# Kernel optimization log

Measured on AMD Instinct MI355X. Metric: run time of the kernel, lower is better.

The kernel has to match this reference:

```python
import jax, jax.numpy as jnp
import numpy as np

B, N, NBR, C = 1, 2048, 32, 384
C1, OUT = 32, 128


def setup_inputs() -> dict:
    key = jax.random.key(0)
    ks = jax.random.split(key, 6)
    return {
        "s_i": jax.random.normal(ks[0], (B, N, C), dtype=jnp.float32),
        "s_j": jax.random.normal(ks[1], (B, N, NBR, C), dtype=jnp.float32),
        "m_i": jnp.ones((B, N), dtype=jnp.float32),
        "m_j": jnp.ones((B, N, NBR), dtype=jnp.float32),
        "Wl": jax.random.normal(ks[2], (C, C1), dtype=jnp.float32) * (C ** -0.5),
        "bl": jnp.zeros((C1,), dtype=jnp.float32),
        "Wr": jax.random.normal(ks[3], (C, C1), dtype=jnp.float32) * (C ** -0.5),
        "br": jnp.zeros((C1,), dtype=jnp.float32),
        "Wo": jax.random.normal(ks[4], (C1 * C1, OUT), dtype=jnp.float32) * ((C1 * C1) ** -0.5),
        "bo": jnp.zeros((OUT,), dtype=jnp.float32),
    }


def reference(s_i, s_j, m_i, m_j, Wl, bl, Wr, br, Wo, bo):
    # Masked projections
    left = m_i[..., None] * (jnp.einsum('bic,ca->bia', s_i, Wl) + bl)      # (B, N, C1)
    right = m_j[..., None] * (jnp.einsum('bikc,ca->bika', s_j, Wr) + br)   # (B, N, n, C1)
    # Per-(residue, neighbor) outer product; equals the repeat/reshape/transpose
    # dance in the original: out[b,i,k,a*C1+c] = left[b,i,a] * right[b,i,k,c]
    op = jnp.einsum('bia,bikc->bikac', left, right)                        # (B, N, n, C1, C1)
    b_, n_, k_ = op.shape[:3]
    op = op.reshape(b_, n_, k_, C1 * C1)
    # Output projection
    return jnp.einsum('bikd,do->biko', op, Wo) + bo                        # (B, N, n, OUT)
```

## Files before the change

### kernel.cpp

```cpp
#include <hip/hip_runtime.h>

constexpr int NRES = 2048;
constexpr int NBR  = 32;
constexpr int C    = 384;
constexpr int C1   = 32;
constexpr int OUTD = 128;

constexpr int CHUNK = 64;
constexpr int NCH   = C / CHUNK;
constexpr int SJ_LD = CHUNK + 4;

__global__ __launch_bounds__(256, 4) void outerprod_kernel(
    const float* __restrict__ s_i, const float* __restrict__ s_j,
    const float* __restrict__ m_i, const float* __restrict__ m_j,
    const float* __restrict__ Wl,  const float* __restrict__ bl,
    const float* __restrict__ Wr,  const float* __restrict__ br,
    const float* __restrict__ Wo,  const float* __restrict__ bo,
    float* __restrict__ out)
{
    const int i = blockIdx.x;
    const int t = threadIdx.x;

    __shared__ float red[8][C1];
    __shared__ float lft[C1];
    __shared__ float rgt[NBR * C1];
    __shared__ float Tm[C1 * OUTD];
    __shared__ float sj[2][NBR * SJ_LD];

    const int f0 = t,        kk0 = f0 >> 4, c40 = (f0 & 15) * 4;
    const int f1 = t + 256,  kk1 = f1 >> 4, c41 = (f1 & 15) * 4;
    const float* sjbase = s_j + (size_t)i * NBR * C;

    float4 st0 = *reinterpret_cast<const float4*>(sjbase + kk0 * C + c40);
    float4 st1 = *reinterpret_cast<const float4*>(sjbase + kk1 * C + c41);

    {
        const int a = t & 31, g = t >> 5;
        const float* si = s_i + (size_t)i * C;
        const int c0 = g * 48;
        float acc = 0.f;
        #pragma unroll 4
        for (int c = c0; c < c0 + 48; c += 4) {
            const float4 s4 = *reinterpret_cast<const float4*>(si + c);
            acc = fmaf(s4.x, Wl[(c + 0) * C1 + a], acc);
            acc = fmaf(s4.y, Wl[(c + 1) * C1 + a], acc);
            acc = fmaf(s4.z, Wl[(c + 2) * C1 + a], acc);
            acc = fmaf(s4.w, Wl[(c + 3) * C1 + a], acc);
        }
        red[g][a] = acc;
    }
    __syncthreads();

    *reinterpret_cast<float4*>(&sj[0][kk0 * SJ_LD + c40]) = st0;
    *reinterpret_cast<float4*>(&sj[0][kk1 * SJ_LD + c41]) = st1;

    if (t < C1) {
        float acc = bl[t];
        #pragma unroll
        for (int g = 0; g < 8; ++g) acc += red[g][t];
        lft[t] = m_i[i] * acc;
    }

    const int k = t >> 3, cg = t & 7;
    float acc0 = 0.f, acc1 = 0.f, acc2 = 0.f, acc3 = 0.f;
    int cur = 0;
    for (int ch = 0; ch < NCH; ++ch) {
        if (ch + 1 < NCH) {
            st0 = *reinterpret_cast<const float4*>(sjbase + kk0 * C + (ch + 1) * CHUNK + c40);
            st1 = *reinterpret_cast<const float4*>(sjbase + kk1 * C + (ch + 1) * CHUNK + c41);
        }
        __syncthreads();

        const float* srow  = &sj[cur][k * SJ_LD];
        const float* wbase = Wr + (size_t)(ch * CHUNK) * C1 + cg * 4;
        #pragma unroll
        for (int c4 = 0; c4 < CHUNK / 4; ++c4) {
            const float4 s4 = *reinterpret_cast<const float4*>(srow + c4 * 4);
            float4 w;
            w = *reinterpret_cast<const float4*>(wbase + (c4 * 4 + 0) * C1);
            acc0 = fmaf(s4.x, w.x, acc0); acc1 = fmaf(s4.x, w.y, acc1);
            acc2 = fmaf(s4.x, w.z, acc2); acc3 = fmaf(s4.x, w.w, acc3);
            w = *reinterpret_cast<const float4*>(wbase + (c4 * 4 + 1) * C1);
            acc0 = fmaf(s4.y, w.x, acc0); acc1 = fmaf(s4.y, w.y, acc1);
            acc2 = fmaf(s4.y, w.z, acc2); acc3 = fmaf(s4.y, w.w, acc3);
            w = *reinterpret_cast<const float4*>(wbase + (c4 * 4 + 2) * C1);
            acc0 = fmaf(s4.z, w.x, acc0); acc1 = fmaf(s4.z, w.y, acc1);
            acc2 = fmaf(s4.z, w.z, acc2); acc3 = fmaf(s4.z, w.w, acc3);
            w = *reinterpret_cast<const float4*>(wbase + (c4 * 4 + 3) * C1);
            acc0 = fmaf(s4.w, w.x, acc0); acc1 = fmaf(s4.w, w.y, acc1);
            acc2 = fmaf(s4.w, w.z, acc2); acc3 = fmaf(s4.w, w.w, acc3);
        }

        if (ch + 1 < NCH) {
            *reinterpret_cast<float4*>(&sj[cur ^ 1][kk0 * SJ_LD + c40]) = st0;
            *reinterpret_cast<float4*>(&sj[cur ^ 1][kk1 * SJ_LD + c41]) = st1;
        }
        cur ^= 1;
    }
    {
        const float  m  = m_j[i * NBR + k];
        const float4 b4 = *reinterpret_cast<const float4*>(br + cg * 4);
        rgt[k * C1 + cg * 4 + 0] = m * (acc0 + b4.x);
        rgt[k * C1 + cg * 4 + 1] = m * (acc1 + b4.y);
        rgt[k * C1 + cg * 4 + 2] = m * (acc2 + b4.z);
        rgt[k * C1 + cg * 4 + 3] = m * (acc3 + b4.w);
    }
    __syncthreads();

    #pragma unroll
    for (int j = 0; j < 4; ++j) {
        const int e4 = t + j * 256;
        const int c  = e4 >> 5;
        const int o  = (e4 & 31) * 4;
        float a0 = 0.f, a1 = 0.f, a2 = 0.f, a3 = 0.f;
        #pragma unroll 8
        for (int a = 0; a < C1; ++a) {
            const float  l  = lft[a];
            const float4 w4 = *reinterpret_cast<const float4*>(
                Wo + ((size_t)(a * C1 + c)) * OUTD + o);
            a0 = fmaf(l, w4.x, a0); a1 = fmaf(l, w4.y, a1);
            a2 = fmaf(l, w4.z, a2); a3 = fmaf(l, w4.w, a3);
        }
        float4 r = {a0, a1, a2, a3};
        *reinterpret_cast<float4*>(&Tm[c * OUTD + o]) = r;
    }
    __syncthreads();

    #pragma unroll
    for (int j = 0; j < 4; ++j) {
        const int e4 = t + j * 256;
        const int kk = e4 >> 5;
        const int o  = (e4 & 31) * 4;
        const float4 b4 = *reinterpret_cast<const float4*>(bo + o);
        float a0 = b4.x, a1 = b4.y, a2 = b4.z, a3 = b4.w;
        #pragma unroll 8
        for (int c = 0; c < C1; ++c) {
            const float  r  = rgt[kk * C1 + c];
            const float4 tv = *reinterpret_cast<const float4*>(&Tm[c * OUTD + o]);
            a0 = fmaf(r, tv.x, a0); a1 = fmaf(r, tv.y, a1);
            a2 = fmaf(r, tv.z, a2); a3 = fmaf(r, tv.w, a3);
        }
        const float4 res = {a0, a1, a2, a3};
        *reinterpret_cast<float4*>(&out[((size_t)i * NBR + kk) * OUTD + o]) = res;
    }
}

extern "C" void kernel_launch(void* const* d_in, const int* in_sizes, int n_in,
                              void* d_out, int out_size, void* d_ws, size_t ws_size,
                              hipStream_t stream) {
    (void)in_sizes; (void)n_in; (void)out_size; (void)d_ws; (void)ws_size;
    const float* s_i = (const float*)d_in[0];
    const float* s_j = (const float*)d_in[1];
    const float* m_i = (const float*)d_in[2];
    const float* m_j = (const float*)d_in[3];
    const float* Wl  = (const float*)d_in[4];
    const float* bl  = (const float*)d_in[5];
    const float* Wr  = (const float*)d_in[6];
    const float* br  = (const float*)d_in[7];
    const float* Wo  = (const float*)d_in[8];
    const float* bo  = (const float*)d_in[9];
    float* out = (float*)d_out;

    outerprod_kernel<<<NRES, 256, 0, stream>>>(
        s_i, s_j, m_i, m_j, Wl, bl, Wr, br, Wo, bo, out);
}
```

Before: 317.9 us.

## Split fused kernel into projection, T-matrix GEMM, and output kernels via workspace

Replaces the single per-residue fused kernel with three kernels. The first computes the left and right projections over 128-row tiles, using a swizzled shared-memory layout and storing right transposed. The second computes the per-residue T = L·Wo as a register-tiled GEMM so Wo is reused across 64 residues. The third combines R with T to produce the output. The goal is to stop every block re-reading the whole 512KB Wo. The cost is a 32MB T intermediate round-tripped through global memory plus extra launches, and the path depends on the workspace being large enough, with the old kernel kept as a fallback.

```diff
diff --git a/kernel.cpp b/kernel.cpp
--- a/kernel.cpp
+++ b/kernel.cpp
@@ -5,12 +5,181 @@
 constexpr int C    = 384;
 constexpr int C1   = 32;
 constexpr int OUTD = 128;
-
-constexpr int CHUNK = 64;
-constexpr int NCH   = C / CHUNK;
-constexpr int SJ_LD = CHUNK + 4;
-
-__global__ __launch_bounds__(256, 4) void outerprod_kernel(
+constexpr int M1   = NRES * NBR;
+
+constexpr size_t R_OFF = 0;
+constexpr size_t L_OFF = (size_t)8 << 20;
+constexpr size_t T_OFF = (size_t)9 << 20;
+constexpr size_t WS_NEED = T_OFF + (size_t)NRES * (C1 * OUTD) * sizeof(float);
+
+__global__ __launch_bounds__(256) void k1_proj(
+    const float* __restrict__ s_i, const float* __restrict__ s_j,
+    const float* __restrict__ m_i, const float* __restrict__ m_j,
+    const float* __restrict__ Wl,  const float* __restrict__ bl,
+    const float* __restrict__ Wr,  const float* __restrict__ br,
+    float* __restrict__ Rt, float* __restrict__ Lg)
+{
+    const int b    = blockIdx.x;
+    const int t    = threadIdx.x;
+    const int lane = t & 63;
+    const int n0   = __builtin_amdgcn_readfirstlane((t >> 6) * 8);
+
+    __shared__ float sj[128 * 32];
+
+    float4 st[4];
+    #pragma unroll
+    for (int j = 0; j < 4; ++j) {
+        const int idx = t + j * 256, r = idx >> 3, c4 = idx & 7;
+        st[j] = *(const float4*)(s_j + (size_t)(b * 128 + r) * C + c4 * 4);
+    }
+
+    if (t < 128) {
+        const int ii = t >> 5, a = t & 31;
+        const int gi = b * 4 + ii;
+        const float* si = s_i + (size_t)gi * C;
+        float acc = bl[a];
+        #pragma unroll 4
+        for (int c = 0; c < C; c += 4) {
+            const float4 s4 = *(const float4*)(si + c);
+            acc = fmaf(s4.x, Wl[(c + 0) * C1 + a], acc);
+            acc = fmaf(s4.y, Wl[(c + 1) * C1 + a], acc);
+            acc = fmaf(s4.z, Wl[(c + 2) * C1 + a], acc);
+            acc = fmaf(s4.w, Wl[(c + 3) * C1 + a], acc);
+        }
+        Lg[gi * C1 + a] = m_i[gi] * acc;
+    }
+
+    float a0[8], a1[8];
+    #pragma unroll
+    for (int j = 0; j < 8; ++j) { a0[j] = 0.f; a1[j] = 0.f; }
+    const int row0 = lane, row1 = lane + 64;
+    const int sw0 = row0 & 7;
+
+    for (int ch = 0; ch < 12; ++ch) {
+        #pragma unroll
+        for (int j = 0; j < 4; ++j) {
+            const int idx = t + j * 256, r = idx >> 3, c4 = idx & 7;
+            *(float4*)(&sj[r * 32 + ((c4 ^ (r & 7)) << 2)]) = st[j];
+        }
+        if (ch < 11) {
+            #pragma unroll
+            for (int j = 0; j < 4; ++j) {
+                const int idx = t + j * 256, r = idx >> 3, c4 = idx & 7;
+                st[j] = *(const float4*)(s_j + (size_t)(b * 128 + r) * C + (ch + 1) * 32 + c4 * 4);
+            }
+        }
+        __syncthreads();
+
+        #pragma unroll
+        for (int k4 = 0; k4 < 8; ++k4) {
+            const float4 sa0 = *(const float4*)(&sj[row0 * 32 + ((k4 ^ sw0) << 2)]);
+            const float4 sa1 = *(const float4*)(&sj[row1 * 32 + ((k4 ^ sw0) << 2)]);
+            const float s0v[4] = {sa0.x, sa0.y, sa0.z, sa0.w};
+            const float s1v[4] = {sa1.x, sa1.y, sa1.z, sa1.w};
+            #pragma unroll
+            for (int q = 0; q < 4; ++q) {
+                const int kk = ch * 32 + k4 * 4 + q;
+                #pragma unroll
+                for (int j = 0; j < 8; ++j) {
+                    const float w = Wr[kk * C1 + n0 + j];
+                    a0[j] = fmaf(s0v[q], w, a0[j]);
+                    a1[j] = fmaf(s1v[q], w, a1[j]);
+                }
+            }
+        }
+        __syncthreads();
+    }
+
+    const int gr0 = b * 128 + row0, gr1 = b * 128 + row1;
+    const float mj0 = m_j[gr0], mj1 = m_j[gr1];
+    #pragma unroll
+    for (int j = 0; j < 8; ++j) {
+        const float rb = br[n0 + j];
+        Rt[(size_t)(n0 + j) * M1 + gr0] = mj0 * (a0[j] + rb);
+        Rt[(size_t)(n0 + j) * M1 + gr1] = mj1 * (a1[j] + rb);
+    }
+}
+
+__global__ __launch_bounds__(256) void k2_T(
+    const float* __restrict__ Lg, const float* __restrict__ Wo,
+    float* __restrict__ T)
+{
+    const int bi = blockIdx.x >> 3, bn = blockIdx.x & 7;
+    const int t = threadIdx.x, lane = t & 63;
+    const int ibase = __builtin_amdgcn_readfirstlane(bi * 64 + (t >> 6) * 16);
+    const int nlo = bn * 512 + lane * 4;
+    const int nhi = nlo + 256;
+
+    float4 accL[16], accH[16];
+    #pragma unroll
+    for (int ii = 0; ii < 16; ++ii) {
+        accL[ii] = {0.f, 0.f, 0.f, 0.f};
+        accH[ii] = {0.f, 0.f, 0.f, 0.f};
+    }
+
+    #pragma unroll 1
+    for (int a4 = 0; a4 < 8; ++a4) {
+        #pragma unroll
+        for (int q = 0; q < 4; ++q) {
+            const int a = a4 * 4 + q;
+            const float4 w0 = *(const float4*)(Wo + (size_t)a * 4096 + nlo);
+            const float4 w1 = *(const float4*)(Wo + (size_t)a * 4096 + nhi);
+            #pragma unroll
+            for (int ii = 0; ii < 16; ++ii) {
+                const float lv = Lg[(ibase + ii) * C1 + a];
+                accL[ii].x = fmaf(lv, w0.x, accL[ii].x);
+                accL[ii].y = fmaf(lv, w0.y, accL[ii].y);
+                accL[ii].z = fmaf(lv, w0.z, accL[ii].z);
+                accL[ii].w = fmaf(lv, w0.w, accL[ii].w);
+                accH[ii].x = fmaf(lv, w1.x, accH[ii].x);
+                accH[ii].y = fmaf(lv, w1.y, accH[ii].y);
+                accH[ii].z = fmaf(lv, w1.z, accH[ii].z);
+                accH[ii].w = fmaf(lv, w1.w, accH[ii].w);
+            }
+        }
+    }
+    #pragma unroll
+    for (int ii = 0; ii < 16; ++ii) {
+        *(float4*)(T + (size_t)(ibase + ii) * 4096 + nlo) = accL[ii];
+        *(float4*)(T + (size_t)(ibase + ii) * 4096 + nhi) = accH[ii];
+    }
+}
+
+__global__ __launch_bounds__(256) void k3_out(
+    const float* __restrict__ Rt, const float* __restrict__ T,
+    const float* __restrict__ bo, float* __restrict__ out)
+{
+    const int i = blockIdx.x;
+    const int t = threadIdx.x, lane = t & 63;
+    const int k0 = __builtin_amdgcn_readfirstlane((t >> 6) * 8);
+    const int o  = lane * 2;
+    const float* Trow = T + (size_t)i * 4096;
+
+    float accx[8], accy[8];
+    #pragma unroll
+    for (int r = 0; r < 8; ++r) { accx[r] = 0.f; accy[r] = 0.f; }
+
+    #pragma unroll 4
+    for (int c = 0; c < C1; ++c) {
+        const float2 tv = *(const float2*)(Trow + c * OUTD + o);
+        #pragma unroll
+        for (int r = 0; r < 8; ++r) {
+            const float rv = Rt[(size_t)c * M1 + i * NBR + k0 + r];
+            accx[r] = fmaf(rv, tv.x, accx[r]);
+            accy[r] = fmaf(rv, tv.y, accy[r]);
+        }
+    }
+    const float2 b2 = *(const float2*)(bo + o);
+    #pragma unroll
+    for (int r = 0; r < 8; ++r) {
+        const float2 res = {accx[r] + b2.x, accy[r] + b2.y};
+        *(float2*)(out + ((size_t)i * NBR + k0 + r) * OUTD + o) = res;
+    }
+}
+
+constexpr int FCHUNK = 64, FNCH = C / FCHUNK, FSJ_LD = FCHUNK + 4;
+
+__global__ __launch_bounds__(256, 4) void outerprod_fallback(
     const float* __restrict__ s_i, const float* __restrict__ s_j,
     const float* __restrict__ m_i, const float* __restrict__ m_j,
     const float* __restrict__ Wl,  const float* __restrict__ bl,
@@ -20,20 +189,17 @@
 {
     const int i = blockIdx.x;
     const int t = threadIdx.x;
-
     __shared__ float red[8][C1];
     __shared__ float lft[C1];
     __shared__ float rgt[NBR * C1];
     __shared__ float Tm[C1 * OUTD];
-    __shared__ float sj[2][NBR * SJ_LD];
-
-    const int f0 = t,        kk0 = f0 >> 4, c40 = (f0 & 15) * 4;
-    const int f1 = t + 256,  kk1 = f1 >> 4, c41 = (f1 & 15) * 4;
+    __shared__ float sj[2][NBR * FSJ_LD];
+
+    const int f0 = t,       kk0 = f0 >> 4, c40 = (f0 & 15) * 4;
+    const int f1 = t + 256, kk1 = f1 >> 4, c41 = (f1 & 15) * 4;
     const float* sjbase = s_j + (size_t)i * NBR * C;
-
-    float4 st0 = *reinterpret_cast<const float4*>(sjbase + kk0 * C + c40);
-    float4 st1 = *reinterpret_cast<const float4*>(sjbase + kk1 * C + c41);
-
+    float4 st0 = *(const float4*)(sjbase + kk0 * C + c40);
+    float4 st1 = *(const float4*)(sjbase + kk1 * C + c41);
     {
         const int a = t & 31, g = t >> 5;
         const float* si = s_i + (size_t)i * C;
@@ -41,7 +207,7 @@
         float acc = 0.f;
         #pragma unroll 4
         for (int c = c0; c < c0 + 48; c += 4) {
-            const float4 s4 = *reinterpret_cast<const float4*>(si + c);
+            const float4 s4 = *(const float4*)(si + c);
             acc = fmaf(s4.x, Wl[(c + 0) * C1 + a], acc);
             acc = fmaf(s4.y, Wl[(c + 1) * C1 + a], acc);
             acc = fmaf(s4.z, Wl[(c + 2) * C1 + a], acc);
@@ -50,105 +216,97 @@
         red[g][a] = acc;
     }
     __syncthreads();
-
-    *reinterpret_cast<float4*>(&sj[0][kk0 * SJ_LD + c40]) = st0;
-    *reinterpret_cast<float4*>(&sj[0][kk1 * SJ_LD + c41]) = st1;
-
+    *(float4*)(&sj[0][kk0 * FSJ_LD + c40]) = st0;
+    *(float4*)(&sj[0][kk1 * FSJ_LD + c41]) = st1;
     if (t < C1) {
         float acc = bl[t];
         #pragma unroll
         for (int g = 0; g < 8; ++g) acc += red[g][t];
         lft[t] = m_i[i] * acc;
     }
-
     const int k = t >> 3, cg = t & 7;
     float acc0 = 0.f, acc1 = 0.f, acc2 = 0.f, acc3 = 0.f;
     int cur = 0;
-    for (int ch = 0; ch < NCH; ++ch) {
-        if (ch + 1 < NCH) {
-            st0 = *reinterpret_cast<const float4*>(sjbase + kk0 * C + (ch + 1) * CHUNK + c40);
-            st1 = *reinterpret_cast<const float4*>(sjbase + kk1 * C + (ch + 1) * CHUNK + c41);
+    for (int ch = 0; ch < FNCH; ++ch) {
+        if (ch + 1 < FNCH) {
+            st0 = *(const float4*)(sjbase + kk0 * C + (ch + 1) * FCHUNK + c40);
+            st1 = *(const float4*)(sjbase + kk1 * C + (ch + 1) * FCHUNK + c41);
         }
         __syncthreads();
-
-        const float* srow  = &sj[cur][k * SJ_LD];
-        const float* wbase = Wr + (size_t)(ch * CHUNK) * C1 + cg * 4;
-        #pragma unroll
-        for (int c4 = 0; c4 < CHUNK / 4; ++c4) {
-            const float4 s4 = *reinterpret_cast<const float4*>(srow + c4 * 4);
+        const float* srow  = &sj[cur][k * FSJ_LD];
+        const float* wbase = Wr + (size_t)(ch * FCHUNK) * C1 + cg * 4;
+        #pragma unroll
+        for (int c4 = 0; c4 < FCHUNK / 4; ++c4) {
+            const float4 s4 = *(const float4*)(srow + c4 * 4);
             float4 w;
-            w = *reinterpret_cast<const float4*>(wbase + (c4 * 4 + 0) * C1);
+            w = *(const float4*)(wbase + (c4 * 4 + 0) * C1);
             acc0 = fmaf(s4.x, w.x, acc0); acc1 = fmaf(s4.x, w.y, acc1);
             acc2 = fmaf(s4.x, w.z, acc2); acc3 = fmaf(s4.x, w.w, acc3);
-            w = *reinterpret_cast<const float4*>(wbase + (c4 * 4 + 1) * C1);
+            w = *(const float4*)(wbase + (c4 * 4 + 1) * C1);
             acc0 = fmaf(s4.y, w.x, acc0); acc1 = fmaf(s4.y, w.y, acc1);
             acc2 = fmaf(s4.y, w.z, acc2); acc3 = fmaf(s4.y, w.w, acc3);
-            w = *reinterpret_cast<const float4*>(wbase + (c4 * 4 + 2) * C1);
+            w = *(const float4*)(wbase + (c4 * 4 + 2) * C1);
             acc0 = fmaf(s4.z, w.x, acc0); acc1 = fmaf(s4.z, w.y, acc1);
             acc2 = fmaf(s4.z, w.z, acc2); acc3 = fmaf(s4.z, w.w, acc3);
-            w = *reinterpret_cast<const float4*>(wbase + (c4 * 4 + 3) * C1);
+            w = *(const float4*)(wbase + (c4 * 4 + 3) * C1);
             acc0 = fmaf(s4.w, w.x, acc0); acc1 = fmaf(s4.w, w.y, acc1);
             acc2 = fmaf(s4.w, w.z, acc2); acc3 = fmaf(s4.w, w.w, acc3);
         }
-
-        if (ch + 1 < NCH) {
-            *reinterpret_cast<float4*>(&sj[cur ^ 1][kk0 * SJ_LD + c40]) = st0;
-            *reinterpret_cast<float4*>(&sj[cur ^ 1][kk1 * SJ_LD + c41]) = st1;
+        if (ch + 1 < FNCH) {
+            *(float4*)(&sj[cur ^ 1][kk0 * FSJ_LD + c40]) = st0;
+            *(float4*)(&sj[cur ^ 1][kk1 * FSJ_LD + c41]) = st1;
         }
         cur ^= 1;
     }
     {
         const float  m  = m_j[i * NBR + k];
-        const float4 b4 = *reinterpret_cast<const float4*>(br + cg * 4);
+        const float4 b4 = *(const float4*)(br + cg * 4);
         rgt[k * C1 + cg * 4 + 0] = m * (acc0 + b4.x);
         rgt[k * C1 + cg * 4 + 1] = m * (acc1 + b4.y);
         rgt[k * C1 + cg * 4 + 2] = m * (acc2 + b4.z);
         rgt[k * C1 + cg * 4 + 3] = m * (acc3 + b4.w);
     }
     __syncthreads();
-
     #pragma unroll
     for (int j = 0; j < 4; ++j) {
         const int e4 = t + j * 256;
         const int c  = e4 >> 5;
         const int o  = (e4 & 31) * 4;
-        float a0 = 0.f, a1 = 0.f, a2 = 0.f, a3 = 0.f;
+        float x0 = 0.f, x1 = 0.f, x2 = 0.f, x3 = 0.f;
         #pragma unroll 8
         for (int a = 0; a < C1; ++a) {
             const float  l  = lft[a];
-            const float4 w4 = *reinterpret_cast<const float4*>(
-                Wo + ((size_t)(a * C1 + c)) * OUTD + o);
-            a0 = fmaf(l, w4.x, a0); a1 = fmaf(l, w4.y, a1);
-            a2 = fmaf(l, w4.z, a2); a3 = fmaf(l, w4.w, a3);
-        }
-        float4 r = {a0, a1, a2, a3};
-        *reinterpret_cast<float4*>(&Tm[c * OUTD + o]) = r;
+            const float4 w4 = *(const float4*)(Wo + ((size_t)(a * C1 + c)) * OUTD + o);
+            x0 = fmaf(l, w4.x, x0); x1 = fmaf(l, w4.y, x1);
+            x2 = fmaf(l, w4.z, x2); x3 = fmaf(l, w4.w, x3);
+        }
+        float4 r = {x0, x1, x2, x3};
+        *(float4*)(&Tm[c * OUTD + o]) = r;
     }
     __syncthreads();
-
     #pragma unroll
     for (int j = 0; j < 4; ++j) {
         const int e4 = t + j * 256;
         const int kk = e4 >> 5;
         const int o  = (e4 & 31) * 4;
-        const float4 b4 = *reinterpret_cast<const float4*>(bo + o);
-        float a0 = b4.x, a1 = b4.y, a2 = b4.z, a3 = b4.w;
+        const float4 b4 = *(const float4*)(bo + o);
+        float x0 = b4.x, x1 = b4.y, x2 = b4.z, x3 = b4.w;
         #pragma unroll 8
         for (int c = 0; c < C1; ++c) {
             const float  r  = rgt[kk * C1 + c];
-            const float4 tv = *reinterpret_cast<const float4*>(&Tm[c * OUTD + o]);
-            a0 = fmaf(r, tv.x, a0); a1 = fmaf(r, tv.y, a1);
-            a2 = fmaf(r, tv.z, a2); a3 = fmaf(r, tv.w, a3);
-        }
-        const float4 res = {a0, a1, a2, a3};
-        *reinterpret_cast<float4*>(&out[((size_t)i * NBR + kk) * OUTD + o]) = res;
+            const float4 tv = *(const float4*)(&Tm[c * OUTD + o]);
+            x0 = fmaf(r, tv.x, x0); x1 = fmaf(r, tv.y, x1);
+            x2 = fmaf(r, tv.z, x2); x3 = fmaf(r, tv.w, x3);
+        }
+        const float4 res = {x0, x1, x2, x3};
+        *(float4*)(&out[((size_t)i * NBR + kk) * OUTD + o]) = res;
     }
 }
 
 extern "C" void kernel_launch(void* const* d_in, const int* in_sizes, int n_in,
                               void* d_out, int out_size, void* d_ws, size_t ws_size,
                               hipStream_t stream) {
-    (void)in_sizes; (void)n_in; (void)out_size; (void)d_ws; (void)ws_size;
+    (void)in_sizes; (void)n_in; (void)out_size;
     const float* s_i = (const float*)d_in[0];
     const float* s_j = (const float*)d_in[1];
     const float* m_i = (const float*)d_in[2];
@@ -161,6 +319,15 @@
     const float* bo  = (const float*)d_in[9];
     float* out = (float*)d_out;
 
-    outerprod_kernel<<<NRES, 256, 0, stream>>>(
-        s_i, s_j, m_i, m_j, Wl, bl, Wr, br, Wo, bo, out);
-}
+    if (ws_size >= WS_NEED) {
+        float* Rt = (float*)((char*)d_ws + R_OFF);
+        float* Lg = (float*)((char*)d_ws + L_OFF);
+        float* T  = (float*)((char*)d_ws + T_OFF);
+        k1_proj<<<M1 / 128, 256, 0, stream>>>(s_i, s_j, m_i, m_j, Wl, bl, Wr, br, Rt, Lg);
+        k2_T<<<(NRES / 64) * 8, 256, 0, stream>>>(Lg, Wo, T);
+        k3_out<<<NRES, 256, 0, stream>>>(Rt, T, bo, out);
+    } else {
+        outerprod_fallback<<<NRES, 256, 0, stream>>>(
+            s_i, s_j, m_i, m_j, Wl, bl, Wr, br, Wo, bo, out);
+    }
+}
```

New measurement: 281.7 us. 1.13x faster.
